# Performance work log

Hardware: AMD Instinct MI355X
Metric: run time of the kernel (lower is better)

Reference implementation:

```python
import jax, jax.numpy as jnp
import numpy as np

BN_EPS = 1e-5
R = 8.0        # radius
L = 11         # sequence kernel size (odd), s = L//2
K = 24         # kernel_channels[-1]
N_NODES = 32768
N_EDGES = 524288
C_IN = 128     # in_channels == out_channels
C_W = 32       # width = out_channels * base_width / 64


def _bn(x, gamma, beta):
    # BatchNorm1d in training mode: biased batch statistics over node dim
    mu = jnp.mean(x, axis=0)
    var = jnp.mean(jnp.square(x - mu), axis=0)
    return (x - mu) * jax.lax.rsqrt(var + BN_EPS) * gamma + beta


def _lrelu(x, slope):
    return jnp.where(x >= 0, x, slope * x)


def setup_inputs() -> dict:
    key = jax.random.key(0)
    ks = jax.random.split(key, 10)

    def glorot(k, shape, fan_in):
        return jax.random.normal(k, shape, jnp.float32) * np.float32(1.0 / np.sqrt(fan_in))

    inp = {}
    inp["x"] = jax.random.normal(ks[0], (N_NODES, C_IN), jnp.float32)
    inp["pos"] = jax.random.normal(ks[1], (N_NODES, 3), jnp.float32) * 10.0
    inp["ori"] = jax.random.normal(ks[2], (N_NODES, 9), jnp.float32)
    inp["seq"] = jnp.arange(N_NODES, dtype=jnp.int32)
    inp["edge_index"] = jax.random.randint(ks[3], (2, N_EDGES), 0, N_NODES, jnp.int32)
    # input MLP params: BN(C_IN) -> LeakyReLU(0.1) -> Linear(C_IN->C_W, no bias) -> BN(C_W) -> LeakyReLU(0.1)
    inp["bn1_g"] = jnp.ones((C_IN,), jnp.float32)
    inp["bn1_b"] = jnp.zeros((C_IN,), jnp.float32)
    inp["lin1_w"] = glorot(ks[4], (C_IN, C_W), C_IN)
    inp["bn2_g"] = jnp.ones((C_W,), jnp.float32)
    inp["bn2_b"] = jnp.zeros((C_W,), jnp.float32)
    # CDConv WeightNet (single layer kernel_channels=[K]): per-seq-bin affine 7 -> K
    inp["wn_w"] = glorot(ks[5], (L, 7, K), 7)
    inp["wn_b"] = jnp.zeros((L, K), jnp.float32)
    # CDConv output projection: [K*C_W, C_W]
    inp["conv_w"] = glorot(ks[6], (K * C_W, C_W), K * C_W)
    # output Linear: BN(C_W) -> LeakyReLU(0.1) -> Linear(C_W->C_IN, no bias)
    inp["bn3_g"] = jnp.ones((C_W,), jnp.float32)
    inp["bn3_b"] = jnp.zeros((C_W,), jnp.float32)
    inp["lin2_w"] = glorot(ks[7], (C_W, C_IN), C_W)
    return inp


def reference(x, pos, ori, seq, edge_index,
              bn1_g, bn1_b, lin1_w, bn2_g, bn2_b,
              wn_w, wn_b, conv_w, bn3_g, bn3_b, lin2_w):
    n = x.shape[0]
    identity = x  # in_channels == out_channels -> identity branch is passthrough

    # ----- input MLP (mid_channels=None) -----
    h = _lrelu(_bn(x, bn1_g, bn1_b), 0.1)
    h = h @ lin1_w                       # [N, C_W]
    h = _lrelu(_bn(h, bn2_g, bn2_b), 0.1)

    # ----- CDConv: continuous geometric kernel over neighbor edges -----
    src, dst = edge_index[0], edge_index[1]      # message j=src -> i=dst
    d = pos[src] - pos[dst]                      # [E,3]
    dist = jnp.linalg.norm(d, axis=-1, keepdims=True)
    direction = d / (dist + 1e-9)
    Ri = ori[dst].reshape(-1, 3, 3)              # receiver local frame
    Rj = ori[src].reshape(-1, 3, 3)
    pos_local = jnp.einsum('eij,ej->ei', Ri, direction)      # direction in local frame
    ori_feat = jnp.einsum('eij,ej->ei', Ri, Rj[:, 0, :])     # neighbor axis in local frame
    delta = jnp.concatenate([pos_local, ori_feat, dist / R], axis=-1)  # [E,7]

    s = L // 2
    sidx = jnp.clip(seq[src] - seq[dst], -s, s) + s          # [E] in [0, L)

    # WeightNet: per-edge affine selected by sequence bin, LeakyReLU(0.2)
    w = _lrelu(jnp.einsum('ef,efk->ek', delta, wn_w[sidx]) + wn_b[sidx], 0.2)  # [E,K]

    # message = outer(kernel_weight, x_j), scatter-sum to receivers
    msg = (w[:, :, None] * h[src][:, None, :]).reshape(w.shape[0], K * C_W)   # [E, K*C_W]
    agg = jax.ops.segment_sum(msg, dst, num_segments=n)                        # [N, K*C_W]
    h = agg @ conv_w                                                            # [N, C_W]

    # ----- output Linear + residual -----
    h = _lrelu(_bn(h, bn3_g, bn3_b), 0.1)
    out = h @ lin2_w + identity
    return out
```

## Files before the change

kernel.cpp:

```cpp
#include <hip/hip_runtime.h>

#define N_NODES 32768
#define C_IN 128
#define C_W 32
#define KK 24
#define SS 5
#define GG 8
#define AGS (KK * C_W + 4)

__global__ void __launch_bounds__(256) k_pre(
        const float* __restrict__ x, float* __restrict__ s1,
        const int* __restrict__ ei, int E, int* __restrict__ counts) {
    int t = threadIdx.x;
    int c = t % C_IN;
    int r0 = blockIdx.x * 2 + t / C_IN;
    float s = 0.f, sq = 0.f;
    for (int r = r0; r < N_NODES; r += 1024) {
        float v = x[(size_t)r * C_IN + c];
        s += v; sq += v * v;
    }
    atomicAdd(&s1[c], s);
    atomicAdd(&s1[C_IN + c], sq);
    for (int e = blockIdx.x * 256 + t; e < E; e += 512 * 256)
        atomicAdd(&counts[ei[E + e]], 1);
}

__global__ void __launch_bounds__(256) k_mlp1(
        const float* __restrict__ x, const float* __restrict__ s1,
        const float* __restrict__ g1, const float* __restrict__ b1,
        const float* __restrict__ w1, float* __restrict__ hpre,
        float* __restrict__ s2sh) {
    __shared__ float sAB[2][C_IN];
    __shared__ float sx[32][C_IN + 4];
    __shared__ float sw[C_IN][C_W];
    const int t = threadIdx.x;
    const int row0 = blockIdx.x * 32;
    if (t < C_IN) {
        float mean = s1[t] * (1.f / N_NODES);
        float var = s1[C_IN + t] * (1.f / N_NODES) - mean * mean;
        float a = g1[t] * rsqrtf(var + 1e-5f);
        sAB[0][t] = a; sAB[1][t] = b1[t] - mean * a;
    }
    for (int idx = t; idx < C_IN * C_W; idx += 256)
        sw[idx / C_W][idx % C_W] = w1[idx];
    __syncthreads();
    for (int idx = t; idx < 32 * 32; idx += 256) {
        int r = idx >> 5, cq = idx & 31;
        float4 v = *(const float4*)&x[(size_t)(row0 + r) * C_IN + cq * 4];
        float* d = &sx[r][cq * 4];
        float a0 = sAB[0][cq*4+0]*v.x + sAB[1][cq*4+0];
        float a1 = sAB[0][cq*4+1]*v.y + sAB[1][cq*4+1];
        float a2 = sAB[0][cq*4+2]*v.z + sAB[1][cq*4+2];
        float a3 = sAB[0][cq*4+3]*v.w + sAB[1][cq*4+3];
        d[0] = a0 >= 0.f ? a0 : 0.1f * a0;
        d[1] = a1 >= 0.f ? a1 : 0.1f * a1;
        d[2] = a2 >= 0.f ? a2 : 0.1f * a2;
        d[3] = a3 >= 0.f ? a3 : 0.1f * a3;
    }
    __syncthreads();
    const int r = t >> 3, c0 = (t & 7) * 4;
    float ac0 = 0.f, ac1 = 0.f, ac2 = 0.f, ac3 = 0.f;
    #pragma unroll 8
    for (int cc = 0; cc < C_IN; ++cc) {
        float xv = sx[r][cc];
        float4 wv = *(const float4*)&sw[cc][c0];
        ac0 += xv * wv.x; ac1 += xv * wv.y; ac2 += xv * wv.z; ac3 += xv * wv.w;
    }
    float4 o; o.x = ac0; o.y = ac1; o.z = ac2; o.w = ac3;
    *(float4*)&hpre[(size_t)(row0 + r) * C_W + c0] = o;
    __syncthreads();
    sx[r][c0] = ac0; sx[r][c0+1] = ac1; sx[r][c0+2] = ac2; sx[r][c0+3] = ac3;
    __syncthreads();
    if (t < C_W) {
        float s = 0.f, sq = 0.f;
        #pragma unroll
        for (int rr = 0; rr < 32; ++rr) {
            float v = sx[rr][t];
            s += v; sq += v * v;
        }
        int sh = (blockIdx.x & 7) * 64;
        atomicAdd(&s2sh[sh + t], s);
        atomicAdd(&s2sh[sh + C_W + t], sq);
    }
}

__global__ void __launch_bounds__(1024) k_scan(
        const int* __restrict__ counts, int* __restrict__ offsets,
        int* __restrict__ cursor) {
    __shared__ int sblk[1024];
    const int t = threadIdx.x;
    const int base = t * 32;
    const int4* cp = (const int4*)(counts + base);
    int loc[32];
    int s = 0;
    #pragma unroll
    for (int q = 0; q < 8; ++q) {
        int4 v = cp[q];
        loc[q*4+0] = s; s += v.x;
        loc[q*4+1] = s; s += v.y;
        loc[q*4+2] = s; s += v.z;
        loc[q*4+3] = s; s += v.w;
    }
    sblk[t] = s;
    __syncthreads();
    for (int d = 1; d < 1024; d <<= 1) {
        int u = (t >= d) ? sblk[t - d] : 0;
        __syncthreads();
        sblk[t] += u;
        __syncthreads();
    }
    const int blockbase = sblk[t] - s;
    #pragma unroll
    for (int q = 0; q < 8; ++q) {
        int4 o;
        o.x = blockbase + loc[q*4+0];
        o.y = blockbase + loc[q*4+1];
        o.z = blockbase + loc[q*4+2];
        o.w = blockbase + loc[q*4+3];
        ((int4*)(offsets + base))[q] = o;
        ((int4*)(cursor + base))[q] = o;
    }
    if (t == 1023) offsets[N_NODES] = sblk[1023];
}

__global__ void __launch_bounds__(256) k_edge(
        const int* __restrict__ ei, int E,
        const float* __restrict__ pos, const float* __restrict__ ori,
        const int* __restrict__ seq,
        const float* __restrict__ wnw, const float* __restrict__ wnb,
        int* __restrict__ cursor, int* __restrict__ srcPerm,
        float* __restrict__ wPerm) {
    __shared__ float sWnw[11][169];
    __shared__ float sWnb[11][24];
    const int t = threadIdx.x;
    for (int idx = t; idx < 11 * 168; idx += 256)
        sWnw[idx / 168][idx % 168] = wnw[idx];
    for (int idx = t; idx < 11 * 24; idx += 256)
        sWnb[idx / 24][idx % 24] = wnb[idx];
    __syncthreads();
    const int e = blockIdx.x * 256 + t;
    if (e >= E) return;
    const int src = ei[e];
    const int dst = ei[E + e];
    int ds = seq[src] - seq[dst];
    ds = ds < -SS ? -SS : (ds > SS ? SS : ds);
    const int sb = ds + SS;
    float dx = pos[src * 3 + 0] - pos[dst * 3 + 0];
    float dy = pos[src * 3 + 1] - pos[dst * 3 + 1];
    float dz = pos[src * 3 + 2] - pos[dst * 3 + 2];
    float dist = sqrtf(dx * dx + dy * dy + dz * dz);
    float inv = 1.f / (dist + 1e-9f);
    float ux = dx * inv, uy = dy * inv, uz = dz * inv;
    float b0 = ori[src * 9 + 0], b1 = ori[src * 9 + 1], b2 = ori[src * 9 + 2];
    float delta[7];
    #pragma unroll
    for (int r = 0; r < 3; ++r) {
        float m0 = ori[dst * 9 + r * 3 + 0];
        float m1 = ori[dst * 9 + r * 3 + 1];
        float m2 = ori[dst * 9 + r * 3 + 2];
        delta[r]     = m0 * ux + m1 * uy + m2 * uz;
        delta[3 + r] = m0 * b0 + m1 * b1 + m2 * b2;
    }
    delta[6] = dist * 0.125f;
    float w[KK];
    #pragma unroll
    for (int k = 0; k < KK; ++k) {
        float acc = sWnb[sb][k];
        #pragma unroll
        for (int f = 0; f < 7; ++f)
            acc += delta[f] * sWnw[sb][f * 24 + k];
        w[k] = acc >= 0.f ? acc : 0.2f * acc;
    }
    const int p = atomicAdd(&cursor[dst], 1);
    srcPerm[p] = src;
    float4* wp = (float4*)(wPerm + (size_t)p * KK);
    #pragma unroll
    for (int q = 0; q < 6; ++q) {
        float4 o; o.x = w[q*4]; o.y = w[q*4+1]; o.z = w[q*4+2]; o.w = w[q*4+3];
        wp[q] = o;
    }
}

__global__ void __launch_bounds__(512, 4) k_node(
    const int* __restrict__ offsets, const int* __restrict__ srcPerm,
    const float* __restrict__ wPerm, const float* __restrict__ hpre,
    const float* __restrict__ s2sh, const float* __restrict__ g2,
    const float* __restrict__ b2, const float* __restrict__ convw,
    float* __restrict__ convout, float* __restrict__ s3sh) {
    __shared__ float sA2[C_W], sB2[C_W];
    __shared__ int sOff[GG + 1];
    __shared__ float sW[GG][32 * KK];
    __shared__ float sAgg[GG][AGS];
    __shared__ float sRed[8][GG][C_W];
    __shared__ float sRv[GG][C_W], sRq[GG][C_W];
    const int t = threadIdx.x;
    const int i0 = blockIdx.x * GG;
    if (t < C_W) {
        float s = 0.f, sq = 0.f;
        #pragma unroll
        for (int j = 0; j < 8; ++j) {
            s  += s2sh[j * 64 + t];
            sq += s2sh[j * 64 + C_W + t];
        }
        float mean = s * (1.f / N_NODES);
        float var = sq * (1.f / N_NODES) - mean * mean;
        float a = g2[t] * rsqrtf(var + 1e-5f);
        sA2[t] = a; sB2[t] = b2[t] - mean * a;
    }
    if (t <= GG) sOff[t] = offsets[i0 + t];
    __syncthreads();

    const int w    = t >> 6;
    const int lane = t & 63;
    const int c    = lane & 31;
    const int s    = lane >> 5;
    const float bnA = sA2[c], bnB = sB2[c];
    const int beg = sOff[w], end = sOff[w + 1];
    float* sWw = &sW[w][0];
    float a[KK];
    #pragma unroll
    for (int k = 0; k < KK; ++k) a[k] = 0.f;

    for (int cb = beg; cb < end; cb += 32) {
        const int m = min(32, end - cb);
        int srcL = srcPerm[cb + min(c, m - 1)];
        const float4* gsrc = (const float4*)(wPerm + (size_t)cb * KK);
        #pragma unroll
        for (int u = 0; u < 3; ++u) {
            int idx = lane + u * 64;
            if (idx < m * 6) ((float4*)sWw)[idx] = gsrc[idx];
        }
        #pragma unroll 2
        for (int j2 = 0; j2 < m; j2 += 2) {
            const int slot = min(j2 + s, m - 1);
            const bool ok = (j2 + s) < m;
            const int src = __shfl(srcL, slot, 64);
            float h = hpre[(size_t)src * C_W + c];
            float v = bnA * h + bnB;
            v = v >= 0.f ? v : 0.1f * v;
            v = ok ? v : 0.f;
            const float4* wp = (const float4*)(sWw + slot * KK);
            float4 W0 = wp[0], W1 = wp[1], W2 = wp[2];
            float4 W3 = wp[3], W4 = wp[4], W5 = wp[5];
            a[0]  += W0.x * v; a[1]  += W0.y * v; a[2]  += W0.z * v; a[3]  += W0.w * v;
            a[4]  += W1.x * v; a[5]  += W1.y * v; a[6]  += W1.z * v; a[7]  += W1.w * v;
            a[8]  += W2.x * v; a[9]  += W2.y * v; a[10] += W2.z * v; a[11] += W2.w * v;
            a[12] += W3.x * v; a[13] += W3.y * v; a[14] += W3.z * v; a[15] += W3.w * v;
            a[16] += W4.x * v; a[17] += W4.y * v; a[18] += W4.z * v; a[19] += W4.w * v;
            a[20] += W5.x * v; a[21] += W5.y * v; a[22] += W5.z * v; a[23] += W5.w * v;
        }
    }
    #pragma unroll
    for (int k = 0; k < KK; ++k) a[k] += __shfl_xor(a[k], 32, 64);
    if (s == 0) {
        #pragma unroll
        for (int k = 0; k < KK; ++k) sAgg[w][k * C_W + c] = a[k];
    }
    __syncthreads();

    {
        const int coq = t & 7;
        const int gp  = (t >> 3) & 7;
        const int sl8 = t >> 6;
        const int r0  = sl8 * 96;
        float4 acc; acc.x = acc.y = acc.z = acc.w = 0.f;
        #pragma unroll 6
        for (int rc = 0; rc < 96; rc += 4) {
            const float4 s4 = *(const float4*)&sAgg[gp][r0 + rc];
            const float4 w0 = *(const float4*)&convw[(size_t)(r0+rc+0)*32 + coq*4];
            const float4 w1 = *(const float4*)&convw[(size_t)(r0+rc+1)*32 + coq*4];
            const float4 w2 = *(const float4*)&convw[(size_t)(r0+rc+2)*32 + coq*4];
            const float4 w3 = *(const float4*)&convw[(size_t)(r0+rc+3)*32 + coq*4];
            acc.x += s4.x*w0.x + s4.y*w1.x + s4.z*w2.x + s4.w*w3.x;
            acc.y += s4.x*w0.y + s4.y*w1.y + s4.z*w2.y + s4.w*w3.y;
            acc.z += s4.x*w0.z + s4.y*w1.z + s4.z*w2.z + s4.w*w3.z;
            acc.w += s4.x*w0.w + s4.y*w1.w + s4.z*w2.w + s4.w*w3.w;
        }
        *(float4*)&sRed[sl8][gp][coq * 4] = acc;
    }
    __syncthreads();
    if (t < 256) {
        const int gg = t >> 5, co = t & 31;
        float v = 0.f;
        #pragma unroll
        for (int sl = 0; sl < 8; ++sl) v += sRed[sl][gg][co];
        convout[(size_t)(i0 + gg) * C_W + co] = v;
        sRv[gg][co] = v; sRq[gg][co] = v * v;
    }
    __syncthreads();
    if (t < 64) {
        int cc = t & 31;
        bool isq = t >= C_W;
        float s2 = 0.f;
        #pragma unroll
        for (int gg = 0; gg < GG; ++gg)
            s2 += isq ? sRq[gg][cc] : sRv[gg][cc];
        atomicAdd(&s3sh[(blockIdx.x & 7) * 64 + t], s2);
    }
}

__global__ void __launch_bounds__(256) k_out(
        const float* __restrict__ conv, const float* __restrict__ s3sh,
        const float* __restrict__ g3, const float* __restrict__ b3,
        const float* __restrict__ w2, const float* __restrict__ x,
        float* __restrict__ out) {
    __shared__ float sAB[2][C_W];
    __shared__ float sh[8][C_W];
    __shared__ float sw2[C_W][C_IN];
    const int t = threadIdx.x;
    const int row0 = blockIdx.x * 8;
    if (t < C_W) {
        float s = 0.f, sq = 0.f;
        #pragma unroll
        for (int j = 0; j < 8; ++j) {
            s  += s3sh[j * 64 + t];
            sq += s3sh[j * 64 + C_W + t];
        }
        float mean = s * (1.f / N_NODES);
        float var = sq * (1.f / N_NODES) - mean * mean;
        float a = g3[t] * rsqrtf(var + 1e-5f);
        sAB[0][t] = a; sAB[1][t] = b3[t] - mean * a;
    }
    for (int idx = t; idx < C_W * C_IN; idx += 256)
        sw2[idx >> 7][idx & 127] = w2[idx];
    __syncthreads();
    {
        float v = conv[(size_t)row0 * C_W + t];
        int r = t >> 5, cc = t & 31;
        v = sAB[0][cc] * v + sAB[1][cc];
        sh[r][cc] = v >= 0.f ? v : 0.1f * v;
    }
    __syncthreads();
    const int r = t >> 5, c4 = (t & 31) * 4;
    float4 acc = *(const float4*)&x[(size_t)(row0 + r) * C_IN + c4];
    #pragma unroll 8
    for (int cw = 0; cw < C_W; ++cw) {
        float hv = sh[r][cw];
        float4 wv = *(const float4*)&sw2[cw][c4];
        acc.x += hv * wv.x; acc.y += hv * wv.y;
        acc.z += hv * wv.z; acc.w += hv * wv.w;
    }
    *(float4*)&out[(size_t)(row0 + r) * C_IN + c4] = acc;
}

extern "C" void kernel_launch(void* const* d_in, const int* in_sizes, int n_in,
                              void* d_out, int out_size, void* d_ws, size_t ws_size,
                              hipStream_t stream) {
    const float* x     = (const float*)d_in[0];
    const float* pos   = (const float*)d_in[1];
    const float* ori   = (const float*)d_in[2];
    const int*   seq   = (const int*)d_in[3];
    const int*   ei    = (const int*)d_in[4];
    const float* bn1g  = (const float*)d_in[5];
    const float* bn1b  = (const float*)d_in[6];
    const float* lin1w = (const float*)d_in[7];
    const float* bn2g  = (const float*)d_in[8];
    const float* bn2b  = (const float*)d_in[9];
    const float* wnw   = (const float*)d_in[10];
    const float* wnb   = (const float*)d_in[11];
    const float* convw = (const float*)d_in[12];
    const float* bn3g  = (const float*)d_in[13];
    const float* bn3b  = (const float*)d_in[14];
    const float* lin2w = (const float*)d_in[15];
    float* out = (float*)d_out;
    const int E = in_sizes[4] / 2;

    char* wsb = (char*)d_ws;
    size_t off = 0;
    auto alloc = [&](size_t bytes) {
        void* p = wsb + off;
        off = (off + bytes + 255) & ~(size_t)255;
        return p;
    };
    float* s1      = (float*)alloc(256 * 4);
    float* s2sh    = (float*)alloc(512 * 4);
    float* s3sh    = (float*)alloc(512 * 4);
    int*   counts  = (int*)alloc((size_t)N_NODES * 4);
    size_t zero_bytes = off;
    int*   offsets = (int*)alloc(((size_t)N_NODES + 1) * 4);
    int*   cursor  = (int*)alloc((size_t)N_NODES * 4);
    int*   srcPerm = (int*)alloc((size_t)E * 4);
    float* hpre    = (float*)alloc((size_t)N_NODES * C_W * 4);
    float* convo   = (float*)alloc((size_t)N_NODES * C_W * 4);
    float* wPerm   = (float*)alloc((size_t)E * KK * 4);

    hipMemsetAsync(wsb, 0, zero_bytes, stream);

    k_pre<<<512, 256, 0, stream>>>(x, s1, ei, E, counts);
    k_scan<<<1, 1024, 0, stream>>>(counts, offsets, cursor);
    k_edge<<<(E + 255) / 256, 256, 0, stream>>>(ei, E, pos, ori, seq, wnw, wnb,
                                                cursor, srcPerm, wPerm);
    k_mlp1<<<N_NODES / 32, 256, 0, stream>>>(x, s1, bn1g, bn1b, lin1w, hpre, s2sh);
    k_node<<<N_NODES / GG, 512, 0, stream>>>(offsets, srcPerm, wPerm, hpre,
                                             s2sh, bn2g, bn2b, convw, convo, s3sh);
    k_out<<<N_NODES / 8, 256, 0, stream>>>(convo, s3sh, bn3g, bn3b, lin2w, x, out);
}
```

Baseline: 275.2 us.

## Fuse WeightNet edge weights into node aggregation kernel, drop wPerm buffer

Removes the per-edge kernel that computed 24 WeightNet weights and wrote them to a permuted global buffer. The scatter kernel now only builds the CSR source list. Each node kernel recomputes the edge geometry and weights on the fly, with the two half-waves splitting the 24 kernel channels. The weights are staged in LDS as packed bf16, and the 16 source features are gathered up front. This cuts the large wPerm write and read traffic, at the cost of redundant gathers of pos, ori and seq per edge, more register pressure, and reduced precision from rounding the weights to bf16.

```diff
diff --git a/kernel.cpp b/kernel.cpp
--- a/kernel.cpp
+++ b/kernel.cpp
@@ -7,6 +7,8 @@
 #define SS 5
 #define GG 8
 #define AGS (KK * C_W + 4)
+#define WNS 172
+#define WBS 28
 
 __global__ void __launch_bounds__(256) k_pre(
         const float* __restrict__ x, float* __restrict__ s1,
@@ -123,78 +125,42 @@
     if (t == 1023) offsets[N_NODES] = sblk[1023];
 }
 
-__global__ void __launch_bounds__(256) k_edge(
-        const int* __restrict__ ei, int E,
-        const float* __restrict__ pos, const float* __restrict__ ori,
-        const int* __restrict__ seq,
-        const float* __restrict__ wnw, const float* __restrict__ wnb,
-        int* __restrict__ cursor, int* __restrict__ srcPerm,
-        float* __restrict__ wPerm) {
-    __shared__ float sWnw[11][169];
-    __shared__ float sWnb[11][24];
-    const int t = threadIdx.x;
-    for (int idx = t; idx < 11 * 168; idx += 256)
-        sWnw[idx / 168][idx % 168] = wnw[idx];
-    for (int idx = t; idx < 11 * 24; idx += 256)
-        sWnb[idx / 24][idx % 24] = wnb[idx];
-    __syncthreads();
-    const int e = blockIdx.x * 256 + t;
-    if (e >= E) return;
-    const int src = ei[e];
-    const int dst = ei[E + e];
-    int ds = seq[src] - seq[dst];
-    ds = ds < -SS ? -SS : (ds > SS ? SS : ds);
-    const int sb = ds + SS;
-    float dx = pos[src * 3 + 0] - pos[dst * 3 + 0];
-    float dy = pos[src * 3 + 1] - pos[dst * 3 + 1];
-    float dz = pos[src * 3 + 2] - pos[dst * 3 + 2];
-    float dist = sqrtf(dx * dx + dy * dy + dz * dz);
-    float inv = 1.f / (dist + 1e-9f);
-    float ux = dx * inv, uy = dy * inv, uz = dz * inv;
-    float b0 = ori[src * 9 + 0], b1 = ori[src * 9 + 1], b2 = ori[src * 9 + 2];
-    float delta[7];
-    #pragma unroll
-    for (int r = 0; r < 3; ++r) {
-        float m0 = ori[dst * 9 + r * 3 + 0];
-        float m1 = ori[dst * 9 + r * 3 + 1];
-        float m2 = ori[dst * 9 + r * 3 + 2];
-        delta[r]     = m0 * ux + m1 * uy + m2 * uz;
-        delta[3 + r] = m0 * b0 + m1 * b1 + m2 * b2;
-    }
-    delta[6] = dist * 0.125f;
-    float w[KK];
-    #pragma unroll
-    for (int k = 0; k < KK; ++k) {
-        float acc = sWnb[sb][k];
-        #pragma unroll
-        for (int f = 0; f < 7; ++f)
-            acc += delta[f] * sWnw[sb][f * 24 + k];
-        w[k] = acc >= 0.f ? acc : 0.2f * acc;
-    }
-    const int p = atomicAdd(&cursor[dst], 1);
-    srcPerm[p] = src;
-    float4* wp = (float4*)(wPerm + (size_t)p * KK);
-    #pragma unroll
-    for (int q = 0; q < 6; ++q) {
-        float4 o; o.x = w[q*4]; o.y = w[q*4+1]; o.z = w[q*4+2]; o.w = w[q*4+3];
-        wp[q] = o;
+__global__ void __launch_bounds__(256) k_scatter(
+        const int* __restrict__ ei, int E, int* __restrict__ cursor,
+        int* __restrict__ srcPerm) {
+    int e = blockIdx.x * 256 + threadIdx.x;
+    if (e < E) {
+        int dst = ei[E + e];
+        int p = atomicAdd(&cursor[dst], 1);
+        srcPerm[p] = ei[e];
     }
 }
 
 __global__ void __launch_bounds__(512, 4) k_node(
     const int* __restrict__ offsets, const int* __restrict__ srcPerm,
-    const float* __restrict__ wPerm, const float* __restrict__ hpre,
+    const float* __restrict__ pos, const float* __restrict__ ori,
+    const int* __restrict__ seq, const float* __restrict__ hpre,
     const float* __restrict__ s2sh, const float* __restrict__ g2,
-    const float* __restrict__ b2, const float* __restrict__ convw,
+    const float* __restrict__ b2,
+    const float* __restrict__ wnw, const float* __restrict__ wnb,
+    const float* __restrict__ convw,
     float* __restrict__ convout, float* __restrict__ s3sh) {
+
     __shared__ float sA2[C_W], sB2[C_W];
     __shared__ int sOff[GG + 1];
-    __shared__ float sW[GG][32 * KK];
+    __shared__ float sWnw[11 * WNS];
+    __shared__ float sWnb[11 * WBS];
+    __shared__ unsigned int sWp[GG][32 * 16];
     __shared__ float sAgg[GG][AGS];
     __shared__ float sRed[8][GG][C_W];
     __shared__ float sRv[GG][C_W], sRq[GG][C_W];
+
     const int t = threadIdx.x;
     const int i0 = blockIdx.x * GG;
+    for (int idx = t; idx < 11 * 168; idx += 512)
+        sWnw[(idx / 168) * WNS + idx % 168] = wnw[idx];
+    for (int idx = t; idx < 11 * 24; idx += 512)
+        sWnb[(idx / 24) * WBS + idx % 24] = wnb[idx];
     if (t < C_W) {
         float s = 0.f, sq = 0.f;
         #pragma unroll
@@ -210,52 +176,132 @@
     if (t <= GG) sOff[t] = offsets[i0 + t];
     __syncthreads();
 
-    const int w    = t >> 6;
-    const int lane = t & 63;
-    const int c    = lane & 31;
-    const int s    = lane >> 5;
+    const int w = t >> 6, lane = t & 63, c = lane & 31, s = lane >> 5;
+    const int i = i0 + w;
     const float bnA = sA2[c], bnB = sB2[c];
+    const float pi0 = pos[i*3+0], pi1 = pos[i*3+1], pi2 = pos[i*3+2];
+    float Rm[9];
+    #pragma unroll
+    for (int r = 0; r < 9; ++r) Rm[r] = ori[i*9+r];
+    const int si = seq[i];
     const int beg = sOff[w], end = sOff[w + 1];
-    float* sWw = &sW[w][0];
-    float a[KK];
+    unsigned int* sWw = &sWp[w][0];
+    float a[12];
     #pragma unroll
-    for (int k = 0; k < KK; ++k) a[k] = 0.f;
+    for (int j = 0; j < 12; ++j) a[j] = 0.f;
 
     for (int cb = beg; cb < end; cb += 32) {
         const int m = min(32, end - cb);
-        int srcL = srcPerm[cb + min(c, m - 1)];
-        const float4* gsrc = (const float4*)(wPerm + (size_t)cb * KK);
-        #pragma unroll
-        for (int u = 0; u < 3; ++u) {
-            int idx = lane + u * 64;
-            if (idx < m * 6) ((float4*)sWw)[idx] = gsrc[idx];
-        }
-        #pragma unroll 2
-        for (int j2 = 0; j2 < m; j2 += 2) {
-            const int slot = min(j2 + s, m - 1);
-            const bool ok = (j2 + s) < m;
-            const int src = __shfl(srcL, slot, 64);
-            float h = hpre[(size_t)src * C_W + c];
-            float v = bnA * h + bnB;
+        const int src = srcPerm[cb + min(c, m - 1)];
+        float hr[16];
+        #pragma unroll
+        for (int q = 0; q < 16; ++q) {
+            int ee = min(2 * q + s, m - 1);
+            int sq_ = __shfl(src, ee, 32);
+            hr[q] = hpre[(size_t)sq_ * C_W + c];
+        }
+        float px = pos[src*3+0], py = pos[src*3+1], pz = pos[src*3+2];
+        float o0 = ori[src*9+0], o1 = ori[src*9+1], o2 = ori[src*9+2];
+        int sqs = seq[src];
+        float dx = px - pi0, dy = py - pi1, dz = pz - pi2;
+        float dist = sqrtf(dx*dx + dy*dy + dz*dz);
+        float inv = 1.f / (dist + 1e-9f);
+        float ux = dx*inv, uy = dy*inv, uz = dz*inv;
+        float df[7];
+        df[0] = Rm[0]*ux + Rm[1]*uy + Rm[2]*uz;
+        df[1] = Rm[3]*ux + Rm[4]*uy + Rm[5]*uz;
+        df[2] = Rm[6]*ux + Rm[7]*uy + Rm[8]*uz;
+        df[3] = Rm[0]*o0 + Rm[1]*o1 + Rm[2]*o2;
+        df[4] = Rm[3]*o0 + Rm[4]*o1 + Rm[5]*o2;
+        df[5] = Rm[6]*o0 + Rm[7]*o1 + Rm[8]*o2;
+        df[6] = dist * 0.125f;
+        int dsq = sqs - si; dsq = dsq < -SS ? -SS : (dsq > SS ? SS : dsq);
+        const int sb = dsq + SS;
+        float wv[12];
+        {
+            const float* wb = &sWnb[sb * WBS + s * 12];
+            float4 b0 = *(const float4*)&wb[0];
+            float4 b1 = *(const float4*)&wb[4];
+            float4 b2_ = *(const float4*)&wb[8];
+            wv[0]=b0.x; wv[1]=b0.y; wv[2]=b0.z; wv[3]=b0.w;
+            wv[4]=b1.x; wv[5]=b1.y; wv[6]=b1.z; wv[7]=b1.w;
+            wv[8]=b2_.x; wv[9]=b2_.y; wv[10]=b2_.z; wv[11]=b2_.w;
+        }
+        const float* wn = &sWnw[sb * WNS + s * 12];
+        #pragma unroll
+        for (int f = 0; f < 7; ++f) {
+            float4 q0 = *(const float4*)&wn[f*24 + 0];
+            float4 q1 = *(const float4*)&wn[f*24 + 4];
+            float4 q2 = *(const float4*)&wn[f*24 + 8];
+            float d_ = df[f];
+            wv[0]+=d_*q0.x; wv[1]+=d_*q0.y; wv[2]+=d_*q0.z; wv[3]+=d_*q0.w;
+            wv[4]+=d_*q1.x; wv[5]+=d_*q1.y; wv[6]+=d_*q1.z; wv[7]+=d_*q1.w;
+            wv[8]+=d_*q2.x; wv[9]+=d_*q2.y; wv[10]+=d_*q2.z; wv[11]+=d_*q2.w;
+        }
+        #pragma unroll
+        for (int j = 0; j < 12; ++j) wv[j] = wv[j] >= 0.f ? wv[j] : 0.2f * wv[j];
+        unsigned int pk[6];
+        #pragma unroll
+        for (int jj = 0; jj < 6; ++jj) {
+            unsigned int ulo = __float_as_uint(wv[2*jj]);
+            unsigned int uhi = __float_as_uint(wv[2*jj+1]);
+            ulo = (ulo + 0x7FFFu + ((ulo >> 16) & 1u)) >> 16;
+            uhi = (uhi + 0x7FFFu + ((uhi >> 16) & 1u)) & 0xFFFF0000u;
+            pk[jj] = uhi | ulo;
+        }
+        {
+            uint4 w4; w4.x = pk[0]; w4.y = pk[1]; w4.z = pk[2]; w4.w = pk[3];
+            *(uint4*)&sWw[c * 16 + s * 8] = w4;
+            uint2 w2_; w2_.x = pk[4]; w2_.y = pk[5];
+            *(uint2*)&sWw[c * 16 + s * 8 + 4] = w2_;
+        }
+        #pragma unroll
+        for (int q = 0; q < 16; ++q) {
+            float v = bnA * hr[q] + bnB;
             v = v >= 0.f ? v : 0.1f * v;
-            v = ok ? v : 0.f;
-            const float4* wp = (const float4*)(sWw + slot * KK);
-            float4 W0 = wp[0], W1 = wp[1], W2 = wp[2];
-            float4 W3 = wp[3], W4 = wp[4], W5 = wp[5];
-            a[0]  += W0.x * v; a[1]  += W0.y * v; a[2]  += W0.z * v; a[3]  += W0.w * v;
-            a[4]  += W1.x * v; a[5]  += W1.y * v; a[6]  += W1.z * v; a[7]  += W1.w * v;
-            a[8]  += W2.x * v; a[9]  += W2.y * v; a[10] += W2.z * v; a[11] += W2.w * v;
-            a[12] += W3.x * v; a[13] += W3.y * v; a[14] += W3.z * v; a[15] += W3.w * v;
-            a[16] += W4.x * v; a[17] += W4.y * v; a[18] += W4.z * v; a[19] += W4.w * v;
-            a[20] += W5.x * v; a[21] += W5.y * v; a[22] += W5.z * v; a[23] += W5.w * v;
+            hr[q] = (2 * q + s < m) ? v : 0.f;
+        }
+        #pragma unroll
+        for (int q = 0; q < 16; ++q) {
+            float oth = __shfl_xor(hr[q], 32);
+            float v0 = (s == 0) ? hr[q] : oth;
+            float v1 = (s == 0) ? oth : hr[q];
+            {
+                uint4 pA = *(const uint4*)&sWw[(2*q) * 16 + s * 8];
+                uint2 pB = *(const uint2*)&sWw[(2*q) * 16 + s * 8 + 4];
+                a[0]  += __uint_as_float(pA.x << 16) * v0;
+                a[1]  += __uint_as_float(pA.x & 0xFFFF0000u) * v0;
+                a[2]  += __uint_as_float(pA.y << 16) * v0;
+                a[3]  += __uint_as_float(pA.y & 0xFFFF0000u) * v0;
+                a[4]  += __uint_as_float(pA.z << 16) * v0;
+                a[5]  += __uint_as_float(pA.z & 0xFFFF0000u) * v0;
+                a[6]  += __uint_as_float(pA.w << 16) * v0;
+                a[7]  += __uint_as_float(pA.w & 0xFFFF0000u) * v0;
+                a[8]  += __uint_as_float(pB.x << 16) * v0;
+                a[9]  += __uint_as_float(pB.x & 0xFFFF0000u) * v0;
+                a[10] += __uint_as_float(pB.y << 16) * v0;
+                a[11] += __uint_as_float(pB.y & 0xFFFF0000u) * v0;
+            }
+            {
+                uint4 pA = *(const uint4*)&sWw[(2*q+1) * 16 + s * 8];
+                uint2 pB = *(const uint2*)&sWw[(2*q+1) * 16 + s * 8 + 4];
+                a[0]  += __uint_as_float(pA.x << 16) * v1;
+                a[1]  += __uint_as_float(pA.x & 0xFFFF0000u) * v1;
+                a[2]  += __uint_as_float(pA.y << 16) * v1;
+                a[3]  += __uint_as_float(pA.y & 0xFFFF0000u) * v1;
+                a[4]  += __uint_as_float(pA.z << 16) * v1;
+                a[5]  += __uint_as_float(pA.z & 0xFFFF0000u) * v1;
+                a[6]  += __uint_as_float(pA.w << 16) * v1;
+                a[7]  += __uint_as_float(pA.w & 0xFFFF0000u) * v1;
+                a[8]  += __uint_as_float(pB.x << 16) * v1;
+                a[9]  += __uint_as_float(pB.x & 0xFFFF0000u) * v1;
+                a[10] += __uint_as_float(pB.y << 16) * v1;
+                a[11] += __uint_as_float(pB.y & 0xFFFF0000u) * v1;
+            }
         }
     }
     #pragma unroll
-    for (int k = 0; k < KK; ++k) a[k] += __shfl_xor(a[k], 32, 64);
-    if (s == 0) {
-        #pragma unroll
-        for (int k = 0; k < KK; ++k) sAgg[w][k * C_W + c] = a[k];
-    }
+    for (int j = 0; j < 12; ++j) sAgg[w][(s * 12 + j) * C_W + c] = a[j];
     __syncthreads();
 
     {
@@ -382,16 +428,15 @@
     int*   srcPerm = (int*)alloc((size_t)E * 4);
     float* hpre    = (float*)alloc((size_t)N_NODES * C_W * 4);
     float* convo   = (float*)alloc((size_t)N_NODES * C_W * 4);
-    float* wPerm   = (float*)alloc((size_t)E * KK * 4);
 
     hipMemsetAsync(wsb, 0, zero_bytes, stream);
 
     k_pre<<<512, 256, 0, stream>>>(x, s1, ei, E, counts);
     k_scan<<<1, 1024, 0, stream>>>(counts, offsets, cursor);
-    k_edge<<<(E + 255) / 256, 256, 0, stream>>>(ei, E, pos, ori, seq, wnw, wnb,
-                                                cursor, srcPerm, wPerm);
+    k_scatter<<<(E + 255) / 256, 256, 0, stream>>>(ei, E, cursor, srcPerm);
     k_mlp1<<<N_NODES / 32, 256, 0, stream>>>(x, s1, bn1g, bn1b, lin1w, hpre, s2sh);
-    k_node<<<N_NODES / GG, 512, 0, stream>>>(offsets, srcPerm, wPerm, hpre,
-                                             s2sh, bn2g, bn2b, convw, convo, s3sh);
+    k_node<<<N_NODES / GG, 512, 0, stream>>>(offsets, srcPerm, pos, ori, seq,
+                                             hpre, s2sh, bn2g, bn2b, wnw, wnb,
+                                             convw, convo, s3sh);
     k_out<<<N_NODES / 8, 256, 0, stream>>>(convo, s3sh, bn3g, bn3b, lin2w, x, out);
 }
```

After: 587.5 us. +113.5%, slower.

## Store edge weights as packed bf16 and stage block-wide edge tiles in LDS

Applied to the files above, without the earlier changes.

The edge kernel now rounds the 24 per-edge kernel weights to bf16 and packs them two per 32-bit word, halving the wPerm buffer written and read. The node kernel stages a whole block's contiguous edge range (weights plus source indices) into LDS in 256-edge tiles with cooperative loads. It then processes four edge pairs per iteration so more hpre gathers are in flight. The staging buffer shares LDS with the reduction scratch through a union. Costs are reduced precision in the weights and extra block-wide barriers, and the occupancy hint on launch bounds is dropped.

```diff
diff --git a/kernel.cpp b/kernel.cpp
--- a/kernel.cpp
+++ b/kernel.cpp
@@ -7,6 +7,7 @@
 #define SS 5
 #define GG 8
 #define AGS (KK * C_W + 4)
+#define TCAP 256
 
 __global__ void __launch_bounds__(256) k_pre(
         const float* __restrict__ x, float* __restrict__ s1,
@@ -129,7 +130,7 @@
         const int* __restrict__ seq,
         const float* __restrict__ wnw, const float* __restrict__ wnb,
         int* __restrict__ cursor, int* __restrict__ srcPerm,
-        float* __restrict__ wPerm) {
+        unsigned int* __restrict__ wPerm) {
     __shared__ float sWnw[11][169];
     __shared__ float sWnb[11][24];
     const int t = threadIdx.x;
@@ -173,26 +174,40 @@
     }
     const int p = atomicAdd(&cursor[dst], 1);
     srcPerm[p] = src;
-    float4* wp = (float4*)(wPerm + (size_t)p * KK);
-    #pragma unroll
-    for (int q = 0; q < 6; ++q) {
-        float4 o; o.x = w[q*4]; o.y = w[q*4+1]; o.z = w[q*4+2]; o.w = w[q*4+3];
-        wp[q] = o;
-    }
-}
-
-__global__ void __launch_bounds__(512, 4) k_node(
+    unsigned int pk[12];
+    #pragma unroll
+    for (int jj = 0; jj < 12; ++jj) {
+        unsigned int ulo = __float_as_uint(w[2*jj]);
+        unsigned int uhi = __float_as_uint(w[2*jj+1]);
+        ulo = (ulo + 0x7FFFu + ((ulo >> 16) & 1u)) >> 16;
+        uhi = (uhi + 0x7FFFu + ((uhi >> 16) & 1u)) & 0xFFFF0000u;
+        pk[jj] = uhi | ulo;
+    }
+    uint4* wp = (uint4*)(wPerm + (size_t)p * 12);
+    uint4 o0; o0.x = pk[0]; o0.y = pk[1]; o0.z = pk[2]; o0.w = pk[3];
+    uint4 o1; o1.x = pk[4]; o1.y = pk[5]; o1.z = pk[6]; o1.w = pk[7];
+    uint4 o2; o2.x = pk[8]; o2.y = pk[9]; o2.z = pk[10]; o2.w = pk[11];
+    wp[0] = o0; wp[1] = o1; wp[2] = o2;
+}
+
+#define BF_LO(u) __uint_as_float((u) << 16)
+#define BF_HI(u) __uint_as_float((u) & 0xFFFF0000u)
+
+__global__ void __launch_bounds__(512) k_node(
     const int* __restrict__ offsets, const int* __restrict__ srcPerm,
-    const float* __restrict__ wPerm, const float* __restrict__ hpre,
+    const unsigned int* __restrict__ wPerm, const float* __restrict__ hpre,
     const float* __restrict__ s2sh, const float* __restrict__ g2,
     const float* __restrict__ b2, const float* __restrict__ convw,
     float* __restrict__ convout, float* __restrict__ s3sh) {
+
     __shared__ float sA2[C_W], sB2[C_W];
     __shared__ int sOff[GG + 1];
-    __shared__ float sW[GG][32 * KK];
     __shared__ float sAgg[GG][AGS];
-    __shared__ float sRed[8][GG][C_W];
-    __shared__ float sRv[GG][C_W], sRq[GG][C_W];
+    __shared__ union SU {
+        struct { unsigned int w[TCAP * 12]; int src[TCAP]; } stg;
+        struct { float red[8][GG][C_W]; float rv[GG][C_W]; float rq[GG][C_W]; } fin;
+    } U;
+
     const int t = threadIdx.x;
     const int i0 = blockIdx.x * GG;
     if (t < C_W) {
@@ -210,44 +225,61 @@
     if (t <= GG) sOff[t] = offsets[i0 + t];
     __syncthreads();
 
-    const int w    = t >> 6;
-    const int lane = t & 63;
-    const int c    = lane & 31;
-    const int s    = lane >> 5;
+    const int w = t >> 6, lane = t & 63, c = lane & 31, s = lane >> 5;
     const float bnA = sA2[c], bnB = sB2[c];
     const int beg = sOff[w], end = sOff[w + 1];
-    float* sWw = &sW[w][0];
+    const int blkBeg = sOff[0], blkEnd = sOff[GG];
     float a[KK];
     #pragma unroll
     for (int k = 0; k < KK; ++k) a[k] = 0.f;
 
-    for (int cb = beg; cb < end; cb += 32) {
-        const int m = min(32, end - cb);
-        int srcL = srcPerm[cb + min(c, m - 1)];
-        const float4* gsrc = (const float4*)(wPerm + (size_t)cb * KK);
-        #pragma unroll
-        for (int u = 0; u < 3; ++u) {
-            int idx = lane + u * 64;
-            if (idx < m * 6) ((float4*)sWw)[idx] = gsrc[idx];
-        }
-        #pragma unroll 2
-        for (int j2 = 0; j2 < m; j2 += 2) {
-            const int slot = min(j2 + s, m - 1);
-            const bool ok = (j2 + s) < m;
-            const int src = __shfl(srcL, slot, 64);
-            float h = hpre[(size_t)src * C_W + c];
-            float v = bnA * h + bnB;
-            v = v >= 0.f ? v : 0.1f * v;
-            v = ok ? v : 0.f;
-            const float4* wp = (const float4*)(sWw + slot * KK);
-            float4 W0 = wp[0], W1 = wp[1], W2 = wp[2];
-            float4 W3 = wp[3], W4 = wp[4], W5 = wp[5];
-            a[0]  += W0.x * v; a[1]  += W0.y * v; a[2]  += W0.z * v; a[3]  += W0.w * v;
-            a[4]  += W1.x * v; a[5]  += W1.y * v; a[6]  += W1.z * v; a[7]  += W1.w * v;
-            a[8]  += W2.x * v; a[9]  += W2.y * v; a[10] += W2.z * v; a[11] += W2.w * v;
-            a[12] += W3.x * v; a[13] += W3.y * v; a[14] += W3.z * v; a[15] += W3.w * v;
-            a[16] += W4.x * v; a[17] += W4.y * v; a[18] += W4.z * v; a[19] += W4.w * v;
-            a[20] += W5.x * v; a[21] += W5.y * v; a[22] += W5.z * v; a[23] += W5.w * v;
+    for (int base = blkBeg; base < blkEnd; base += TCAP) {
+        const int cnt = min(TCAP, blkEnd - base);
+        __syncthreads();
+        {
+            const uint4* gw = (const uint4*)(wPerm + (size_t)base * 12);
+            uint4* lw = (uint4*)U.stg.w;
+            for (int u = t; u < cnt * 3; u += 512) lw[u] = gw[u];
+            if (t < cnt) U.stg.src[t] = srcPerm[base + t];
+        }
+        __syncthreads();
+        const int lo = max(beg, base) - base;
+        const int hi = min(end, base + cnt) - base;
+        for (int j8 = lo; j8 < hi; j8 += 8) {
+            const int last = hi - 1;
+            const int e0 = j8 + 0 + s, e1 = j8 + 2 + s;
+            const int e2 = j8 + 4 + s, e3 = j8 + 6 + s;
+            const int s0 = U.stg.src[min(e0, last)];
+            const int s1 = U.stg.src[min(e1, last)];
+            const int s2_ = U.stg.src[min(e2, last)];
+            const int s3_ = U.stg.src[min(e3, last)];
+            float h0 = hpre[(size_t)s0 * C_W + c];
+            float h1 = hpre[(size_t)s1 * C_W + c];
+            float h2 = hpre[(size_t)s2_ * C_W + c];
+            float h3 = hpre[(size_t)s3_ * C_W + c];
+            h0 = bnA*h0 + bnB; h0 = h0 >= 0.f ? h0 : 0.1f*h0; h0 = (e0 < hi) ? h0 : 0.f;
+            h1 = bnA*h1 + bnB; h1 = h1 >= 0.f ? h1 : 0.1f*h1; h1 = (e1 < hi) ? h1 : 0.f;
+            h2 = bnA*h2 + bnB; h2 = h2 >= 0.f ? h2 : 0.1f*h2; h2 = (e2 < hi) ? h2 : 0.f;
+            h3 = bnA*h3 + bnB; h3 = h3 >= 0.f ? h3 : 0.1f*h3; h3 = (e3 < hi) ? h3 : 0.f;
+            #pragma unroll
+            for (int q = 0; q < 4; ++q) {
+                const float v = q == 0 ? h0 : (q == 1 ? h1 : (q == 2 ? h2 : h3));
+                const int ee = min(j8 + 2 * q + s, last);
+                const uint4* wp = (const uint4*)&U.stg.w[ee * 12];
+                const uint4 A = wp[0], B = wp[1], Cc = wp[2];
+                a[0]  += BF_LO(A.x) * v;  a[1]  += BF_HI(A.x) * v;
+                a[2]  += BF_LO(A.y) * v;  a[3]  += BF_HI(A.y) * v;
+                a[4]  += BF_LO(A.z) * v;  a[5]  += BF_HI(A.z) * v;
+                a[6]  += BF_LO(A.w) * v;  a[7]  += BF_HI(A.w) * v;
+                a[8]  += BF_LO(B.x) * v;  a[9]  += BF_HI(B.x) * v;
+                a[10] += BF_LO(B.y) * v;  a[11] += BF_HI(B.y) * v;
+                a[12] += BF_LO(B.z) * v;  a[13] += BF_HI(B.z) * v;
+                a[14] += BF_LO(B.w) * v;  a[15] += BF_HI(B.w) * v;
+                a[16] += BF_LO(Cc.x) * v; a[17] += BF_HI(Cc.x) * v;
+                a[18] += BF_LO(Cc.y) * v; a[19] += BF_HI(Cc.y) * v;
+                a[20] += BF_LO(Cc.z) * v; a[21] += BF_HI(Cc.z) * v;
+                a[22] += BF_LO(Cc.w) * v; a[23] += BF_HI(Cc.w) * v;
+            }
         }
     }
     #pragma unroll
@@ -276,16 +308,16 @@
             acc.z += s4.x*w0.z + s4.y*w1.z + s4.z*w2.z + s4.w*w3.z;
             acc.w += s4.x*w0.w + s4.y*w1.w + s4.z*w2.w + s4.w*w3.w;
         }
-        *(float4*)&sRed[sl8][gp][coq * 4] = acc;
+        *(float4*)&U.fin.red[sl8][gp][coq * 4] = acc;
     }
     __syncthreads();
     if (t < 256) {
         const int gg = t >> 5, co = t & 31;
         float v = 0.f;
         #pragma unroll
-        for (int sl = 0; sl < 8; ++sl) v += sRed[sl][gg][co];
+        for (int sl = 0; sl < 8; ++sl) v += U.fin.red[sl][gg][co];
         convout[(size_t)(i0 + gg) * C_W + co] = v;
-        sRv[gg][co] = v; sRq[gg][co] = v * v;
+        U.fin.rv[gg][co] = v; U.fin.rq[gg][co] = v * v;
     }
     __syncthreads();
     if (t < 64) {
@@ -294,7 +326,7 @@
         float s2 = 0.f;
         #pragma unroll
         for (int gg = 0; gg < GG; ++gg)
-            s2 += isq ? sRq[gg][cc] : sRv[gg][cc];
+            s2 += isq ? U.fin.rq[gg][cc] : U.fin.rv[gg][cc];
         atomicAdd(&s3sh[(blockIdx.x & 7) * 64 + t], s2);
     }
 }
@@ -382,7 +414,7 @@
     int*   srcPerm = (int*)alloc((size_t)E * 4);
     float* hpre    = (float*)alloc((size_t)N_NODES * C_W * 4);
     float* convo   = (float*)alloc((size_t)N_NODES * C_W * 4);
-    float* wPerm   = (float*)alloc((size_t)E * KK * 4);
+    unsigned int* wPerm = (unsigned int*)alloc((size_t)E * 12 * 4);
 
     hipMemsetAsync(wsb, 0, zero_bytes, stream);
 
```

Measured after the change: 310.2 us. +12.7%, slower.
